# Performance work log

Hardware: AMD Instinct MI355X
Metric: run time of the kernel (lower is better)

## Reference

```python
import jax, jax.numpy as jnp
import numpy as np

B, T, I, H = 64, 256, 1024, 512


def _gru_layer(x, w_ih, w_hh, b_ih, b_hh):
    """PyTorch-semantics GRU layer, batch_first, h0=0.
    x: [B, T, In]; w_ih: [3H, In]; w_hh: [3H, H]; biases: [3H].
    Gate order (torch): r, z, n.
    """
    h_dim = w_hh.shape[1]
    # precompute input projections for all timesteps: [B, T, 3H]
    gx = jnp.einsum('bti,gi->btg', x, w_ih) + b_ih

    def step(h, gx_t):
        gh = h @ w_hh.T + b_hh                      # [B, 3H]
        xr, xz, xn = jnp.split(gx_t, 3, axis=-1)
        hr, hz, hn = jnp.split(gh, 3, axis=-1)
        r = jax.nn.sigmoid(xr + hr)
        z = jax.nn.sigmoid(xz + hz)
        n = jnp.tanh(xn + r * hn)
        h_new = (1.0 - z) * n + z * h
        return h_new, h_new

    h0 = jnp.zeros((x.shape[0], h_dim), x.dtype)
    _, out = jax.lax.scan(step, h0, jnp.swapaxes(gx, 0, 1))  # out: [T, B, H]
    return jnp.swapaxes(out, 0, 1)                            # [B, T, H]


def setup_inputs() -> dict:
    key = jax.random.key(0)
    ks = jax.random.split(key, 9)
    s1 = 1.0 / np.sqrt(H)   # torch GRU init: U(-1/sqrt(H), 1/sqrt(H)) of layer's hidden
    s2 = 1.0 / np.sqrt(I)
    u = lambda k, shp, s: jax.random.uniform(k, shp, jnp.float32, -s, s)
    return {
        'x': jax.random.normal(ks[0], (B, T, I), jnp.float32),
        'w_ih1': u(ks[1], (3 * H, I), s1),
        'w_hh1': u(ks[2], (3 * H, H), s1),
        'b_ih1': u(ks[3], (3 * H,), s1),
        'b_hh1': u(ks[4], (3 * H,), s1),
        'w_ih2': u(ks[5], (3 * I, H), s2),
        'w_hh2': u(ks[6], (3 * I, I), s2),
        'b_ih2': u(ks[7], (3 * I,), s2),
        'b_hh2': u(ks[8], (3 * I,), s2),
    }


def reference(x, w_ih1, w_hh1, b_ih1, b_hh1, w_ih2, w_hh2, b_ih2, b_hh2):
    h1 = _gru_layer(x, w_ih1, w_hh1, b_ih1, b_hh1)   # [B, T, H]
    h1 = jax.nn.relu(h1)
    out = _gru_layer(h1, w_ih2, w_hh2, b_ih2, b_hh2)  # [B, T, I]
    return out
```

## Files before the change

kernel.cpp:

```cpp
#include <hip/hip_runtime.h>

typedef _Float16 half_t;
typedef _Float16 half8  __attribute__((ext_vector_type(8)));
typedef _Float16 half4v __attribute__((ext_vector_type(4)));
typedef float    f32x4  __attribute__((ext_vector_type(4)));
typedef int      i32x4  __attribute__((ext_vector_type(4)));

#define NB 64
#define NT 256
#define NI 1024
#define NH 512

__device__ __forceinline__ void gload16_cc(i32x4& v, const void* p) {
    asm volatile("global_load_dwordx4 %0, %1, off sc0 sc1"
                 : "=v"(v) : "v"(p) : "memory");
}
__device__ __forceinline__ void gstore16_cc(void* p, i32x4 v) {
    asm volatile("global_store_dwordx4 %0, %1, off sc0 sc1"
                 :: "v"(p), "v"(v) : "memory");
}

__device__ __forceinline__ void flag_barrier(unsigned* slots, int nslots,
                                             int my, unsigned gen, int tid) {
    if (tid < 64) {
        asm volatile("s_waitcnt vmcnt(0)" ::: "memory");
        if (tid == 0) {
            unsigned gv = gen;
            asm volatile("global_store_dword %0, %1, off sc0 sc1"
                         :: "v"(slots + my), "v"(gv) : "memory");
        }
        const unsigned* p = slots + (tid & (nslots - 1));
        int guard = 0;
        while (true) {
            unsigned v;
            asm volatile("global_load_dword %0, %1, off sc0 sc1"
                         : "=v"(v) : "v"(p) : "memory");
            asm volatile("s_waitcnt vmcnt(0)" ::: "memory");
            if (__all(v >= gen)) break;
            __builtin_amdgcn_s_sleep(1);
            if (++guard > (1 << 22)) break;
        }
    }
    __syncthreads();
}

__global__ __launch_bounds__(256) void k_cvt(const float* __restrict__ s,
                                             half_t* __restrict__ d, int n4) {
    int i = blockIdx.x * 256 + threadIdx.x;
    if (i < n4) {
        float4 v = reinterpret_cast<const float4*>(s)[i];
        half4v h;
        h[0] = (half_t)v.x; h[1] = (half_t)v.y; h[2] = (half_t)v.z; h[3] = (half_t)v.w;
        reinterpret_cast<half4v*>(d)[i] = h;
    }
}

template <int K>
__global__ __launch_bounds__(256) void k_gemm(const half_t* __restrict__ A,
                                              const half_t* __restrict__ Bw,
                                              const float* __restrict__ bias,
                                              half_t* __restrict__ C, int N) {
    constexpr int BK = 64;
    __shared__ half_t Al[2][128 * BK] __attribute__((aligned(16)));
    __shared__ half_t Bl[2][128 * BK] __attribute__((aligned(16)));

    const int tid = threadIdx.x, lane = tid & 63, wv = tid >> 6;
    const long m0 = (long)blockIdx.y * 128;
    const long n0 = (long)blockIdx.x * 128;
    const int wm = (wv >> 1) * 64, wn = (wv & 1) * 64;

    f32x4 acc[4][4];
#pragma unroll
    for (int nt = 0; nt < 4; ++nt) {
        float bv = bias[n0 + wn + nt * 16 + (lane & 15)];
#pragma unroll
        for (int mt = 0; mt < 4; ++mt) acc[mt][nt] = (f32x4){bv, bv, bv, bv};
    }

    auto stage = [&](int buf, int kt) {
#pragma unroll
        for (int j = 0; j < 4; ++j) {
            int c = tid + 256 * j;
            int row = c >> 3, cin = c & 7;
            int dst = row * BK + ((cin ^ (row & 7)) << 3);
            *reinterpret_cast<int4*>(&Al[buf][dst]) =
                *reinterpret_cast<const int4*>(A + (m0 + row) * K + kt * BK + cin * 8);
            *reinterpret_cast<int4*>(&Bl[buf][dst]) =
                *reinterpret_cast<const int4*>(Bw + (n0 + row) * K + kt * BK + cin * 8);
        }
    };

    stage(0, 0);
    __syncthreads();
    constexpr int NK = K / BK;
    int buf = 0;
    for (int kt = 0; kt < NK; ++kt) {
        if (kt + 1 < NK) stage(buf ^ 1, kt + 1);
        half8 af[4][2], bf[4][2];
#pragma unroll
        for (int mt = 0; mt < 4; ++mt)
#pragma unroll
            for (int ks = 0; ks < 2; ++ks) {
                int lr = wm + mt * 16 + (lane & 15);
                int off = lr * BK + ((ks * 32 + 8 * (lane >> 4)) ^ ((lr & 7) << 3));
                af[mt][ks] = *reinterpret_cast<const half8*>(&Al[buf][off]);
            }
#pragma unroll
        for (int nt = 0; nt < 4; ++nt)
#pragma unroll
            for (int ks = 0; ks < 2; ++ks) {
                int lr = wn + nt * 16 + (lane & 15);
                int off = lr * BK + ((ks * 32 + 8 * (lane >> 4)) ^ ((lr & 7) << 3));
                bf[nt][ks] = *reinterpret_cast<const half8*>(&Bl[buf][off]);
            }
#pragma unroll
        for (int mt = 0; mt < 4; ++mt)
#pragma unroll
            for (int nt = 0; nt < 4; ++nt)
#pragma unroll
                for (int ks = 0; ks < 2; ++ks)
                    acc[mt][nt] = __builtin_amdgcn_mfma_f32_16x16x32_f16(
                        af[mt][ks], bf[nt][ks], acc[mt][nt], 0, 0, 0);
        __syncthreads();
        buf ^= 1;
    }
#pragma unroll
    for (int mt = 0; mt < 4; ++mt)
#pragma unroll
        for (int nt = 0; nt < 4; ++nt)
#pragma unroll
            for (int i = 0; i < 4; ++i) {
                long row = m0 + wm + mt * 16 + 4 * (lane >> 4) + i;
                long col = n0 + wn + nt * 16 + (lane & 15);
                C[row * N + col] = (half_t)acc[mt][nt][i];
            }
}

__global__ __launch_bounds__(256, 1) void k_phase1(const half_t* __restrict__ whh,
                                                   const float* __restrict__ bhh,
                                                   const half_t* __restrict__ gx,
                                                   half_t* __restrict__ hrelu,
                                                   half_t* __restrict__ hf16,
                                                   unsigned* __restrict__ slots) {
    __shared__ half_t wl[48 * NH] __attribute__((aligned(16)));
    __shared__ half_t hl[16 * NH] __attribute__((aligned(16)));
    __shared__ float xch[3][8][16];
    __shared__ half_t hstore[8][16] __attribute__((aligned(16)));

    const int tid = threadIdx.x, lane = tid & 63, wv = tid >> 6;
    const int g = blockIdx.x & 7, memb = blockIdx.x >> 3;
    const int e0 = memb * 16;
    unsigned* gslots = slots + g * 64;

#pragma unroll
    for (int j = 0; j < 12; ++j) {
        int c = tid + 256 * j;
        int lr = c >> 6, cin = c & 63;
        int grow = (lr >> 4) * NH + e0 + (lr & 15);
        int dst = lr * NH + ((cin ^ (lr & 7)) << 3);
        *reinterpret_cast<int4*>(&wl[dst]) =
            *reinterpret_cast<const int4*>(whh + (long)grow * NH + cin * 8);
    }
#pragma unroll
    for (int j = 0; j < 2; ++j) {
        int c = tid + 256 * j;
        int lr = 8 + (c >> 6), cin = c & 63;
        int4 z; z.x = z.y = z.z = z.w = 0;
        *reinterpret_cast<int4*>(&hl[lr * NH + cin * 8]) = z;
    }
    if (tid < 16) {
        i32x4 z = (i32x4){0, 0, 0, 0};
        int b = tid >> 1, seg = tid & 1;
        gstore16_cc(hf16 + (g * 8 + b) * NH + e0 + seg * 8, z);
    }
    float hp = 0.f;
    __syncthreads();
    flag_barrier(gslots, 32, memb, 1, tid);

    const float bgate = (wv < 3) ? bhh[wv * NH + e0 + (lane & 15)] : 0.f;
    const int b = tid >> 4, e = tid & 15;

    for (int t = 0; t < NT; ++t) {
        const half_t* hsrc = hf16 + (t & 1) * (NB * NH);
        i32x4 sv[2];
#pragma unroll
        for (int j = 0; j < 2; ++j) {
            int c = tid + 256 * j;
            int lr = c >> 6, cin = c & 63;
            gload16_cc(sv[j], hsrc + (g * 8 + lr) * NH + cin * 8);
        }
        float xr = 0.f, xz = 0.f, xn = 0.f;
        long rowbase = 0;
        if (tid < 128) {
            rowbase = (long)(g * 8 + b) * NT + t;
            long gbase = rowbase * (3 * NH) + e0 + e;
            xr = (float)gx[gbase];
            xz = (float)gx[gbase + NH];
            xn = (float)gx[gbase + 2 * NH];
        }
        asm volatile("s_waitcnt vmcnt(0)" ::: "memory");
#pragma unroll
        for (int j = 0; j < 2; ++j) {
            int c = tid + 256 * j;
            int lr = c >> 6, cin = c & 63;
            *reinterpret_cast<i32x4*>(&hl[lr * NH + ((cin ^ (lr & 7)) << 3)]) = sv[j];
        }
        __syncthreads();

        if (wv < 3) {
            f32x4 a0 = (f32x4){bgate, bgate, bgate, bgate};
            f32x4 a1 = (f32x4){0.f, 0.f, 0.f, 0.f};
#pragma unroll
            for (int ks = 0; ks < 16; ks += 2) {
                int ar = lane & 15;
                int br = wv * 16 + (lane & 15);
                int ao0 = ar * NH + ((ks * 32 + 8 * (lane >> 4)) ^ ((ar & 7) << 3));
                int bo0 = br * NH + ((ks * 32 + 8 * (lane >> 4)) ^ ((br & 7) << 3));
                int ao1 = ar * NH + (((ks + 1) * 32 + 8 * (lane >> 4)) ^ ((ar & 7) << 3));
                int bo1 = br * NH + (((ks + 1) * 32 + 8 * (lane >> 4)) ^ ((br & 7) << 3));
                a0 = __builtin_amdgcn_mfma_f32_16x16x32_f16(
                    *reinterpret_cast<const half8*>(&hl[ao0]),
                    *reinterpret_cast<const half8*>(&wl[bo0]), a0, 0, 0, 0);
                a1 = __builtin_amdgcn_mfma_f32_16x16x32_f16(
                    *reinterpret_cast<const half8*>(&hl[ao1]),
                    *reinterpret_cast<const half8*>(&wl[bo1]), a1, 0, 0, 0);
            }
            f32x4 acc = a0 + a1;
            if (lane < 32) {
#pragma unroll
                for (int i = 0; i < 4; ++i)
                    xch[wv][4 * (lane >> 4) + i][lane & 15] = acc[i];
            }
        }
        __syncthreads();

        if (tid < 128) {
            float r = 1.f / (1.f + __expf(-(xr + xch[0][b][e])));
            float z = 1.f / (1.f + __expf(-(xz + xch[1][b][e])));
            float n = tanhf(xn + r * xch[2][b][e]);
            float hn = (1.f - z) * n + z * hp;
            hp = hn;
            hrelu[rowbase * NH + e0 + e] = (half_t)fmaxf(hn, 0.f);
            hstore[b][e] = (half_t)hn;
        }
        __syncthreads();

        if (t + 1 < NT) {
            if (tid < 16) {
                int bb = tid >> 1, seg = tid & 1;
                i32x4 v = *reinterpret_cast<const i32x4*>(&hstore[bb][seg * 8]);
                gstore16_cc(hf16 + ((t + 1) & 1) * (NB * NH) + (g * 8 + bb) * NH + e0 + seg * 8, v);
            }
            flag_barrier(gslots, 32, memb, t + 2, tid);
        }
    }
}

__global__ __launch_bounds__(256, 1) void k_phase2(const half_t* __restrict__ whh,
                                                   const float* __restrict__ bhh,
                                                   const half_t* __restrict__ gx,
                                                   float* __restrict__ out,
                                                   half_t* __restrict__ hf16,
                                                   unsigned* __restrict__ slots) {
    __shared__ half_t wl[48 * NI] __attribute__((aligned(16)));
    __shared__ half_t hl[16 * NI] __attribute__((aligned(16)));
    __shared__ float xch[3][16][16];
    __shared__ half_t hstore[16][16] __attribute__((aligned(16)));

    const int tid = threadIdx.x, lane = tid & 63, wv = tid >> 6;
    const int xcd = blockIdx.x & 7;
    const int g = xcd >> 1;
    const int memb = ((blockIdx.x >> 3) << 1) | (xcd & 1);
    const int e0 = memb * 16;
    unsigned* gslots = slots + g * 64;

#pragma unroll
    for (int j = 0; j < 24; ++j) {
        int c = tid + 256 * j;
        int lr = c >> 7, cin = c & 127;
        int grow = (lr >> 4) * NI + e0 + (lr & 15);
        int dst = lr * NI + ((cin ^ (lr & 7)) << 3);
        *reinterpret_cast<int4*>(&wl[dst]) =
            *reinterpret_cast<const int4*>(whh + (long)grow * NI + cin * 8);
    }
    if (tid < 32) {
        i32x4 z = (i32x4){0, 0, 0, 0};
        int b = tid >> 1, seg = tid & 1;
        gstore16_cc(hf16 + (g * 16 + b) * NI + e0 + seg * 8, z);
    }
    float hp = 0.f;
    __syncthreads();
    flag_barrier(gslots, 64, memb, 1, tid);

    const float bgate = (wv < 3) ? bhh[wv * NI + e0 + (lane & 15)] : 0.f;
    const int b = tid >> 4, e = tid & 15;

    for (int t = 0; t < NT; ++t) {
        const half_t* hsrc = hf16 + (t & 1) * (NB * NI);
        i32x4 sv[8];
#pragma unroll
        for (int j = 0; j < 8; ++j) {
            int c = tid + 256 * j;
            int lr = c >> 7, cin = c & 127;
            gload16_cc(sv[j], hsrc + (g * 16 + lr) * NI + cin * 8);
        }
        long rowbase = (long)(g * 16 + b) * NT + t;
        long gbase = rowbase * (3 * NI) + e0 + e;
        float xr = (float)gx[gbase];
        float xz = (float)gx[gbase + NI];
        float xn = (float)gx[gbase + 2 * NI];
        asm volatile("s_waitcnt vmcnt(0)" ::: "memory");
#pragma unroll
        for (int j = 0; j < 8; ++j) {
            int c = tid + 256 * j;
            int lr = c >> 7, cin = c & 127;
            *reinterpret_cast<i32x4*>(&hl[lr * NI + ((cin ^ (lr & 7)) << 3)]) = sv[j];
        }
        __syncthreads();

        if (wv < 3) {
            f32x4 a0 = (f32x4){bgate, bgate, bgate, bgate};
            f32x4 a1 = (f32x4){0.f, 0.f, 0.f, 0.f};
#pragma unroll
            for (int ks = 0; ks < 32; ks += 2) {
                int ar = lane & 15;
                int br = wv * 16 + (lane & 15);
                int ao0 = ar * NI + ((ks * 32 + 8 * (lane >> 4)) ^ ((ar & 7) << 3));
                int bo0 = br * NI + ((ks * 32 + 8 * (lane >> 4)) ^ ((br & 7) << 3));
                int ao1 = ar * NI + (((ks + 1) * 32 + 8 * (lane >> 4)) ^ ((ar & 7) << 3));
                int bo1 = br * NI + (((ks + 1) * 32 + 8 * (lane >> 4)) ^ ((br & 7) << 3));
                a0 = __builtin_amdgcn_mfma_f32_16x16x32_f16(
                    *reinterpret_cast<const half8*>(&hl[ao0]),
                    *reinterpret_cast<const half8*>(&wl[bo0]), a0, 0, 0, 0);
                a1 = __builtin_amdgcn_mfma_f32_16x16x32_f16(
                    *reinterpret_cast<const half8*>(&hl[ao1]),
                    *reinterpret_cast<const half8*>(&wl[bo1]), a1, 0, 0, 0);
            }
            f32x4 acc = a0 + a1;
#pragma unroll
            for (int i = 0; i < 4; ++i)
                xch[wv][4 * (lane >> 4) + i][lane & 15] = acc[i];
        }
        __syncthreads();

        {
            float r = 1.f / (1.f + __expf(-(xr + xch[0][b][e])));
            float z = 1.f / (1.f + __expf(-(xz + xch[1][b][e])));
            float n = tanhf(xn + r * xch[2][b][e]);
            float hn = (1.f - z) * n + z * hp;
            hp = hn;
            out[rowbase * NI + e0 + e] = hn;
            hstore[b][e] = (half_t)hn;
        }
        __syncthreads();

        if (t + 1 < NT) {
            if (tid < 32) {
                int bb = tid >> 1, seg = tid & 1;
                i32x4 v = *reinterpret_cast<const i32x4*>(&hstore[bb][seg * 8]);
                gstore16_cc(hf16 + ((t + 1) & 1) * (NB * NI) + (g * 16 + bb) * NI + e0 + seg * 8, v);
            }
            flag_barrier(gslots, 64, memb, t + 2, tid);
        }
    }
}

extern "C" void kernel_launch(void* const* d_in, const int* in_sizes, int n_in,
                              void* d_out, int out_size, void* d_ws, size_t ws_size,
                              hipStream_t stream) {
    const float* x     = (const float*)d_in[0];
    const float* w_ih1 = (const float*)d_in[1];
    const float* w_hh1 = (const float*)d_in[2];
    const float* b_ih1 = (const float*)d_in[3];
    const float* b_hh1 = (const float*)d_in[4];
    const float* w_ih2 = (const float*)d_in[5];
    const float* w_hh2 = (const float*)d_in[6];
    const float* b_ih2 = (const float*)d_in[7];
    const float* b_hh2 = (const float*)d_in[8];

    char* ws = (char*)d_ws;
    unsigned* slots1 = (unsigned*)ws;
    unsigned* slots2 = (unsigned*)(ws + 2048);
    half_t* h1f16  = (half_t*)(ws + 4096);
    half_t* h2f16  = (half_t*)(ws + 266240);
    half_t* wih1h  = (half_t*)(ws + 1048576);
    half_t* whh1h  = (half_t*)(ws + 4194304);
    half_t* wih2h  = (half_t*)(ws + 5767168);
    half_t* whh2h  = (half_t*)(ws + 8912896);
    half_t* xh     = (half_t*)(ws + 16777216);
    half_t* hrelu  = (half_t*)(ws + 16777216);
    half_t* gx1    = (half_t*)(ws + 50331648);
    half_t* gx2    = (half_t*)(ws + 50331648);
    float*  out    = (float*)d_out;

    hipMemsetAsync(ws, 0, 4096, stream);

    k_cvt<<<16384, 256, 0, stream>>>(x,     xh,    4194304);
    k_cvt<<<1536,  256, 0, stream>>>(w_ih1, wih1h, 393216);
    k_cvt<<<768,   256, 0, stream>>>(w_hh1, whh1h, 196608);
    k_cvt<<<1536,  256, 0, stream>>>(w_ih2, wih2h, 393216);
    k_cvt<<<3072,  256, 0, stream>>>(w_hh2, whh2h, 786432);

    k_gemm<1024><<<dim3(12, 128), 256, 0, stream>>>(xh, wih1h, b_ih1, gx1, 1536);
    k_phase1<<<256, 256, 0, stream>>>(whh1h, b_hh1, gx1, hrelu, h1f16, slots1);
    k_gemm<512><<<dim3(24, 128), 256, 0, stream>>>(hrelu, wih2h, b_ih2, gx2, 3072);
    k_phase2<<<256, 256, 0, stream>>>(whh2h, b_hh2, gx2, out, h2f16, slots2);
}
```

Measured before the change: 2.139 ms.

## Fuse layer-2 input projection into layer-1 recurrence and convert x inside GEMM

The separate x conversion kernel is removed. The first GEMM now reads fp32 x and converts it to fp16 while staging tiles into shared memory. The layer-2 input projection GEMM and the relu buffer are removed: in phase1 the otherwise idle fourth wave applies relu to the previous step's hidden state and multiplies it by a per-block slice of w_ih2, writing gx2 into a shared buffer that aliases gx1. Both recurrent kernels now prefetch the next step's gate inputs, and phase2 moves its output store between the flag release and the wait. This removes kernel launches and the hrelu round trip, but adds per-step work and LDS use to the latency-bound recurrence, and relies on in-place aliasing of gx1 and gx2 being safe.

```diff
diff --git a/kernel.cpp b/kernel.cpp
--- a/kernel.cpp
+++ b/kernel.cpp
@@ -2,7 +2,6 @@
 
 typedef _Float16 half_t;
 typedef _Float16 half8  __attribute__((ext_vector_type(8)));
-typedef _Float16 half4v __attribute__((ext_vector_type(4)));
 typedef float    f32x4  __attribute__((ext_vector_type(4)));
 typedef int      i32x4  __attribute__((ext_vector_type(4)));
 
@@ -49,17 +48,16 @@
     int i = blockIdx.x * 256 + threadIdx.x;
     if (i < n4) {
         float4 v = reinterpret_cast<const float4*>(s)[i];
-        half4v h;
-        h[0] = (half_t)v.x; h[1] = (half_t)v.y; h[2] = (half_t)v.z; h[3] = (half_t)v.w;
-        reinterpret_cast<half4v*>(d)[i] = h;
-    }
-}
-
-template <int K>
-__global__ __launch_bounds__(256) void k_gemm(const half_t* __restrict__ A,
+        half_t h4[4] = {(half_t)v.x, (half_t)v.y, (half_t)v.z, (half_t)v.w};
+        *reinterpret_cast<long*>(&d[i * 4]) = *reinterpret_cast<long*>(h4);
+    }
+}
+
+template <int K, bool AF32>
+__global__ __launch_bounds__(256) void k_gemm(const void* __restrict__ Av,
                                               const half_t* __restrict__ Bw,
                                               const float* __restrict__ bias,
-                                              half_t* __restrict__ C, int N) {
+                                              half_t* __restrict__ C, int N, int ldc) {
     constexpr int BK = 64;
     __shared__ half_t Al[2][128 * BK] __attribute__((aligned(16)));
     __shared__ half_t Bl[2][128 * BK] __attribute__((aligned(16)));
@@ -83,8 +81,20 @@
             int c = tid + 256 * j;
             int row = c >> 3, cin = c & 7;
             int dst = row * BK + ((cin ^ (row & 7)) << 3);
-            *reinterpret_cast<int4*>(&Al[buf][dst]) =
-                *reinterpret_cast<const int4*>(A + (m0 + row) * K + kt * BK + cin * 8);
+            if constexpr (AF32) {
+                const float* Af = (const float*)Av;
+                const float* src = Af + (m0 + row) * K + kt * BK + cin * 8;
+                float4 f0 = *reinterpret_cast<const float4*>(src);
+                float4 f1 = *reinterpret_cast<const float4*>(src + 4);
+                half8 h;
+                h[0] = (half_t)f0.x; h[1] = (half_t)f0.y; h[2] = (half_t)f0.z; h[3] = (half_t)f0.w;
+                h[4] = (half_t)f1.x; h[5] = (half_t)f1.y; h[6] = (half_t)f1.z; h[7] = (half_t)f1.w;
+                *reinterpret_cast<half8*>(&Al[buf][dst]) = h;
+            } else {
+                const half_t* Ah = (const half_t*)Av;
+                *reinterpret_cast<int4*>(&Al[buf][dst]) =
+                    *reinterpret_cast<const int4*>(Ah + (m0 + row) * K + kt * BK + cin * 8);
+            }
             *reinterpret_cast<int4*>(&Bl[buf][dst]) =
                 *reinterpret_cast<const int4*>(Bw + (n0 + row) * K + kt * BK + cin * 8);
         }
@@ -132,20 +142,26 @@
             for (int i = 0; i < 4; ++i) {
                 long row = m0 + wm + mt * 16 + 4 * (lane >> 4) + i;
                 long col = n0 + wn + nt * 16 + (lane & 15);
-                C[row * N + col] = (half_t)acc[mt][nt][i];
-            }
-}
+                C[row * (long)ldc + col] = (half_t)acc[mt][nt][i];
+            }
+}
+
+#define XCH(gt, bb, ee) xch[((gt) * 8 + (bb)) * 16 + (ee)]
 
 __global__ __launch_bounds__(256, 1) void k_phase1(const half_t* __restrict__ whh,
                                                    const float* __restrict__ bhh,
-                                                   const half_t* __restrict__ gx,
-                                                   half_t* __restrict__ hrelu,
+                                                   const half_t* gx,
+                                                   const half_t* __restrict__ wih2,
+                                                   const float* __restrict__ bih2,
+                                                   half_t* gx2,
                                                    half_t* __restrict__ hf16,
                                                    unsigned* __restrict__ slots) {
-    __shared__ half_t wl[48 * NH] __attribute__((aligned(16)));
-    __shared__ half_t hl[16 * NH] __attribute__((aligned(16)));
-    __shared__ float xch[3][8][16];
-    __shared__ half_t hstore[8][16] __attribute__((aligned(16)));
+    __shared__ __attribute__((aligned(16))) char arena[163840];
+    half_t* wl  = (half_t*)arena;
+    half_t* wl2 = (half_t*)(arena + 49152);
+    half_t* hl  = (half_t*)(arena + 147456);
+    float*  xch = (float*)(arena + 147456 + 8192);
+    half_t* hst = (half_t*)(arena + 147456 + 8192 + 1536);
 
     const int tid = threadIdx.x, lane = tid & 63, wv = tid >> 6;
     const int g = blockIdx.x & 7, memb = blockIdx.x >> 3;
@@ -162,23 +178,37 @@
             *reinterpret_cast<const int4*>(whh + (long)grow * NH + cin * 8);
     }
 #pragma unroll
-    for (int j = 0; j < 2; ++j) {
+    for (int j = 0; j < 24; ++j) {
         int c = tid + 256 * j;
-        int lr = 8 + (c >> 6), cin = c & 63;
-        int4 z; z.x = z.y = z.z = z.w = 0;
-        *reinterpret_cast<int4*>(&hl[lr * NH + cin * 8]) = z;
+        int lr = c >> 6, cin = c & 63;
+        int dst = lr * NH + ((cin ^ (lr & 7)) << 3);
+        *reinterpret_cast<int4*>(&wl2[dst]) =
+            *reinterpret_cast<const int4*>(wih2 + (long)(memb * 96 + lr) * NH + cin * 8);
     }
     if (tid < 16) {
         i32x4 z = (i32x4){0, 0, 0, 0};
-        int b = tid >> 1, seg = tid & 1;
-        gstore16_cc(hf16 + (g * 8 + b) * NH + e0 + seg * 8, z);
+        int bb = tid >> 1, seg = tid & 1;
+        gstore16_cc(hf16 + (g * 8 + bb) * NH + e0 + seg * 8, z);
     }
     float hp = 0.f;
     __syncthreads();
     flag_barrier(gslots, 32, memb, 1, tid);
 
     const float bgate = (wv < 3) ? bhh[wv * NH + e0 + (lane & 15)] : 0.f;
+    float bg2[6];
+    if (wv == 3) {
+#pragma unroll
+        for (int nt2 = 0; nt2 < 6; ++nt2)
+            bg2[nt2] = bih2[memb * 96 + nt2 * 16 + (lane & 15)];
+    }
     const int b = tid >> 4, e = tid & 15;
+    const long rb0 = (long)(g * 8 + b) * NT;
+
+    float xr = 0.f, xz = 0.f, xn = 0.f, nxr = 0.f, nxz = 0.f, nxn = 0.f;
+    if (tid < 128) {
+        long gb = rb0 * 3072 + e0 + e;
+        xr = (float)gx[gb]; xz = (float)gx[gb + NH]; xn = (float)gx[gb + 2 * NH];
+    }
 
     for (int t = 0; t < NT; ++t) {
         const half_t* hsrc = hf16 + (t & 1) * (NB * NH);
@@ -189,15 +219,6 @@
             int lr = c >> 6, cin = c & 63;
             gload16_cc(sv[j], hsrc + (g * 8 + lr) * NH + cin * 8);
         }
-        float xr = 0.f, xz = 0.f, xn = 0.f;
-        long rowbase = 0;
-        if (tid < 128) {
-            rowbase = (long)(g * 8 + b) * NT + t;
-            long gbase = rowbase * (3 * NH) + e0 + e;
-            xr = (float)gx[gbase];
-            xz = (float)gx[gbase + NH];
-            xn = (float)gx[gbase + 2 * NH];
-        }
         asm volatile("s_waitcnt vmcnt(0)" ::: "memory");
 #pragma unroll
         for (int j = 0; j < 2; ++j) {
@@ -206,6 +227,11 @@
             *reinterpret_cast<i32x4*>(&hl[lr * NH + ((cin ^ (lr & 7)) << 3)]) = sv[j];
         }
         __syncthreads();
+
+        if (tid < 128 && t + 1 < NT) {
+            long gb = (rb0 + t + 1) * 3072 + e0 + e;
+            nxr = (float)gx[gb]; nxz = (float)gx[gb + NH]; nxn = (float)gx[gb + 2 * NH];
+        }
 
         if (wv < 3) {
             f32x4 a0 = (f32x4){bgate, bgate, bgate, bgate};
@@ -229,29 +255,111 @@
             if (lane < 32) {
 #pragma unroll
                 for (int i = 0; i < 4; ++i)
-                    xch[wv][4 * (lane >> 4) + i][lane & 15] = acc[i];
+                    XCH(wv, 4 * (lane >> 4) + i, lane & 15) = acc[i];
+            }
+        } else if (t > 0) {
+            f32x4 g2[6];
+#pragma unroll
+            for (int nt2 = 0; nt2 < 6; ++nt2)
+                g2[nt2] = (f32x4){bg2[nt2], bg2[nt2], bg2[nt2], bg2[nt2]};
+#pragma unroll
+            for (int ks = 0; ks < 16; ++ks) {
+                int ar = lane & 15;
+                int ao = ar * NH + ((ks * 32 + 8 * (lane >> 4)) ^ ((ar & 7) << 3));
+                half8 a = *reinterpret_cast<const half8*>(&hl[ao]);
+#pragma unroll
+                for (int j2 = 0; j2 < 8; ++j2)
+                    a[j2] = a[j2] > (half_t)0.f ? a[j2] : (half_t)0.f;
+#pragma unroll
+                for (int nt2 = 0; nt2 < 6; ++nt2) {
+                    int br2 = nt2 * 16 + (lane & 15);
+                    int bo = br2 * NH + ((ks * 32 + 8 * (lane >> 4)) ^ ((br2 & 7) << 3));
+                    g2[nt2] = __builtin_amdgcn_mfma_f32_16x16x32_f16(
+                        a, *reinterpret_cast<const half8*>(&wl2[bo]), g2[nt2], 0, 0, 0);
+                }
+            }
+            if (lane < 32) {
+                int r0 = 4 * (lane >> 4);
+#pragma unroll
+                for (int nt2 = 0; nt2 < 6; ++nt2)
+#pragma unroll
+                    for (int i = 0; i < 4; ++i) {
+                        long bb = g * 8 + r0 + i;
+                        gx2[(bb * NT + (t - 1)) * 3072 + memb * 96 + nt2 * 16 + (lane & 15)] =
+                            (half_t)g2[nt2][i];
+                    }
             }
         }
         __syncthreads();
 
         if (tid < 128) {
-            float r = 1.f / (1.f + __expf(-(xr + xch[0][b][e])));
-            float z = 1.f / (1.f + __expf(-(xz + xch[1][b][e])));
-            float n = tanhf(xn + r * xch[2][b][e]);
+            float r = 1.f / (1.f + __expf(-(xr + XCH(0, b, e))));
+            float z = 1.f / (1.f + __expf(-(xz + XCH(1, b, e))));
+            float n = tanhf(xn + r * XCH(2, b, e));
             float hn = (1.f - z) * n + z * hp;
             hp = hn;
-            hrelu[rowbase * NH + e0 + e] = (half_t)fmaxf(hn, 0.f);
-            hstore[b][e] = (half_t)hn;
-        }
-        __syncthreads();
-
-        if (t + 1 < NT) {
-            if (tid < 16) {
-                int bb = tid >> 1, seg = tid & 1;
-                i32x4 v = *reinterpret_cast<const i32x4*>(&hstore[bb][seg * 8]);
-                gstore16_cc(hf16 + ((t + 1) & 1) * (NB * NH) + (g * 8 + bb) * NH + e0 + seg * 8, v);
-            }
-            flag_barrier(gslots, 32, memb, t + 2, tid);
+            hst[b * 16 + e] = (half_t)hn;
+        }
+        __syncthreads();
+
+        if (tid < 16) {
+            int bb = tid >> 1, seg = tid & 1;
+            i32x4 v = *reinterpret_cast<const i32x4*>(&hst[bb * 16 + seg * 8]);
+            gstore16_cc(hf16 + ((t + 1) & 1) * (NB * NH) + (g * 8 + bb) * NH + e0 + seg * 8, v);
+        }
+        flag_barrier(gslots, 32, memb, t + 2, tid);
+        xr = nxr; xz = nxz; xn = nxn;
+    }
+
+    {
+        const half_t* hsrc = hf16 + (NT & 1) * (NB * NH);
+        i32x4 sv[2];
+#pragma unroll
+        for (int j = 0; j < 2; ++j) {
+            int c = tid + 256 * j;
+            int lr = c >> 6, cin = c & 63;
+            gload16_cc(sv[j], hsrc + (g * 8 + lr) * NH + cin * 8);
+        }
+        asm volatile("s_waitcnt vmcnt(0)" ::: "memory");
+#pragma unroll
+        for (int j = 0; j < 2; ++j) {
+            int c = tid + 256 * j;
+            int lr = c >> 6, cin = c & 63;
+            *reinterpret_cast<i32x4*>(&hl[lr * NH + ((cin ^ (lr & 7)) << 3)]) = sv[j];
+        }
+        __syncthreads();
+        if (wv == 3) {
+            f32x4 g2[6];
+#pragma unroll
+            for (int nt2 = 0; nt2 < 6; ++nt2)
+                g2[nt2] = (f32x4){bg2[nt2], bg2[nt2], bg2[nt2], bg2[nt2]};
+#pragma unroll
+            for (int ks = 0; ks < 16; ++ks) {
+                int ar = lane & 15;
+                int ao = ar * NH + ((ks * 32 + 8 * (lane >> 4)) ^ ((ar & 7) << 3));
+                half8 a = *reinterpret_cast<const half8*>(&hl[ao]);
+#pragma unroll
+                for (int j2 = 0; j2 < 8; ++j2)
+                    a[j2] = a[j2] > (half_t)0.f ? a[j2] : (half_t)0.f;
+#pragma unroll
+                for (int nt2 = 0; nt2 < 6; ++nt2) {
+                    int br2 = nt2 * 16 + (lane & 15);
+                    int bo = br2 * NH + ((ks * 32 + 8 * (lane >> 4)) ^ ((br2 & 7) << 3));
+                    g2[nt2] = __builtin_amdgcn_mfma_f32_16x16x32_f16(
+                        a, *reinterpret_cast<const half8*>(&wl2[bo]), g2[nt2], 0, 0, 0);
+                }
+            }
+            if (lane < 32) {
+                int r0 = 4 * (lane >> 4);
+#pragma unroll
+                for (int nt2 = 0; nt2 < 6; ++nt2)
+#pragma unroll
+                    for (int i = 0; i < 4; ++i) {
+                        long bb = g * 8 + r0 + i;
+                        gx2[(bb * NT + (NT - 1)) * 3072 + memb * 96 + nt2 * 16 + (lane & 15)] =
+                            (half_t)g2[nt2][i];
+                    }
+            }
         }
     }
 }
@@ -264,8 +372,8 @@
                                                    unsigned* __restrict__ slots) {
     __shared__ half_t wl[48 * NI] __attribute__((aligned(16)));
     __shared__ half_t hl[16 * NI] __attribute__((aligned(16)));
-    __shared__ float xch[3][16][16];
-    __shared__ half_t hstore[16][16] __attribute__((aligned(16)));
+    __shared__ float xch2[3][16][16];
+    __shared__ half_t hst[16][16] __attribute__((aligned(16)));
 
     const int tid = threadIdx.x, lane = tid & 63, wv = tid >> 6;
     const int xcd = blockIdx.x & 7;
@@ -285,8 +393,8 @@
     }
     if (tid < 32) {
         i32x4 z = (i32x4){0, 0, 0, 0};
-        int b = tid >> 1, seg = tid & 1;
-        gstore16_cc(hf16 + (g * 16 + b) * NI + e0 + seg * 8, z);
+        int bb = tid >> 1, seg = tid & 1;
+        gstore16_cc(hf16 + (g * 16 + bb) * NI + e0 + seg * 8, z);
     }
     float hp = 0.f;
     __syncthreads();
@@ -294,6 +402,13 @@
 
     const float bgate = (wv < 3) ? bhh[wv * NI + e0 + (lane & 15)] : 0.f;
     const int b = tid >> 4, e = tid & 15;
+    const long rb0 = (long)(g * 16 + b) * NT;
+
+    float xr, xz, xn, nxr = 0.f, nxz = 0.f, nxn = 0.f;
+    {
+        long gb = rb0 * 3072 + e0 + e;
+        xr = (float)gx[gb]; xz = (float)gx[gb + NI]; xn = (float)gx[gb + 2 * NI];
+    }
 
     for (int t = 0; t < NT; ++t) {
         const half_t* hsrc = hf16 + (t & 1) * (NB * NI);
@@ -304,11 +419,6 @@
             int lr = c >> 7, cin = c & 127;
             gload16_cc(sv[j], hsrc + (g * 16 + lr) * NI + cin * 8);
         }
-        long rowbase = (long)(g * 16 + b) * NT + t;
-        long gbase = rowbase * (3 * NI) + e0 + e;
-        float xr = (float)gx[gbase];
-        float xz = (float)gx[gbase + NI];
-        float xn = (float)gx[gbase + 2 * NI];
         asm volatile("s_waitcnt vmcnt(0)" ::: "memory");
 #pragma unroll
         for (int j = 0; j < 8; ++j) {
@@ -317,6 +427,11 @@
             *reinterpret_cast<i32x4*>(&hl[lr * NI + ((cin ^ (lr & 7)) << 3)]) = sv[j];
         }
         __syncthreads();
+
+        if (t + 1 < NT) {
+            long gb = (rb0 + t + 1) * 3072 + e0 + e;
+            nxr = (float)gx[gb]; nxz = (float)gx[gb + NI]; nxn = (float)gx[gb + 2 * NI];
+        }
 
         if (wv < 3) {
             f32x4 a0 = (f32x4){bgate, bgate, bgate, bgate};
@@ -339,29 +454,54 @@
             f32x4 acc = a0 + a1;
 #pragma unroll
             for (int i = 0; i < 4; ++i)
-                xch[wv][4 * (lane >> 4) + i][lane & 15] = acc[i];
-        }
-        __syncthreads();
-
+                xch2[wv][4 * (lane >> 4) + i][lane & 15] = acc[i];
+        }
+        __syncthreads();
+
+        float hn;
         {
-            float r = 1.f / (1.f + __expf(-(xr + xch[0][b][e])));
-            float z = 1.f / (1.f + __expf(-(xz + xch[1][b][e])));
-            float n = tanhf(xn + r * xch[2][b][e]);
-            float hn = (1.f - z) * n + z * hp;
+            float r = 1.f / (1.f + __expf(-(xr + xch2[0][b][e])));
+            float z = 1.f / (1.f + __expf(-(xz + xch2[1][b][e])));
+            float n = tanhf(xn + r * xch2[2][b][e]);
+            hn = (1.f - z) * n + z * hp;
             hp = hn;
-            out[rowbase * NI + e0 + e] = hn;
-            hstore[b][e] = (half_t)hn;
+            hst[b][e] = (half_t)hn;
         }
         __syncthreads();
 
         if (t + 1 < NT) {
             if (tid < 32) {
                 int bb = tid >> 1, seg = tid & 1;
-                i32x4 v = *reinterpret_cast<const i32x4*>(&hstore[bb][seg * 8]);
+                i32x4 v = *reinterpret_cast<const i32x4*>(&hst[bb][seg * 8]);
                 gstore16_cc(hf16 + ((t + 1) & 1) * (NB * NI) + (g * 16 + bb) * NI + e0 + seg * 8, v);
             }
-            flag_barrier(gslots, 64, memb, t + 2, tid);
-        }
+            if (tid < 64) {
+                asm volatile("s_waitcnt vmcnt(0)" ::: "memory");
+                if (tid == 0) {
+                    unsigned gv = t + 2;
+                    asm volatile("global_store_dword %0, %1, off sc0 sc1"
+                                 :: "v"(gslots + memb), "v"(gv) : "memory");
+                }
+            }
+        }
+        out[(rb0 + t) * NI + e0 + e] = hn;
+        if (t + 1 < NT) {
+            if (tid < 64) {
+                const unsigned* p = gslots + (tid & 63);
+                int guard = 0;
+                while (true) {
+                    unsigned v;
+                    asm volatile("global_load_dword %0, %1, off sc0 sc1"
+                                 : "=v"(v) : "v"(p) : "memory");
+                    asm volatile("s_waitcnt vmcnt(0)" ::: "memory");
+                    if (__all(v >= (unsigned)(t + 2))) break;
+                    __builtin_amdgcn_s_sleep(1);
+                    if (++guard > (1 << 22)) break;
+                }
+            }
+            __syncthreads();
+        }
+        xr = nxr; xz = nxz; xn = nxn;
     }
 }
 
@@ -382,27 +522,22 @@
     unsigned* slots1 = (unsigned*)ws;
     unsigned* slots2 = (unsigned*)(ws + 2048);
     half_t* h1f16  = (half_t*)(ws + 4096);
-    half_t* h2f16  = (half_t*)(ws + 266240);
+    half_t* h2f16  = (half_t*)(ws + 135168);
     half_t* wih1h  = (half_t*)(ws + 1048576);
     half_t* whh1h  = (half_t*)(ws + 4194304);
     half_t* wih2h  = (half_t*)(ws + 5767168);
     half_t* whh2h  = (half_t*)(ws + 8912896);
-    half_t* xh     = (half_t*)(ws + 16777216);
-    half_t* hrelu  = (half_t*)(ws + 16777216);
-    half_t* gx1    = (half_t*)(ws + 50331648);
-    half_t* gx2    = (half_t*)(ws + 50331648);
+    half_t* gxU    = (half_t*)(ws + 16777216);
     float*  out    = (float*)d_out;
 
     hipMemsetAsync(ws, 0, 4096, stream);
 
-    k_cvt<<<16384, 256, 0, stream>>>(x,     xh,    4194304);
-    k_cvt<<<1536,  256, 0, stream>>>(w_ih1, wih1h, 393216);
-    k_cvt<<<768,   256, 0, stream>>>(w_hh1, whh1h, 196608);
-    k_cvt<<<1536,  256, 0, stream>>>(w_ih2, wih2h, 393216);
-    k_cvt<<<3072,  256, 0, stream>>>(w_hh2, whh2h, 786432);
-
-    k_gemm<1024><<<dim3(12, 128), 256, 0, stream>>>(xh, wih1h, b_ih1, gx1, 1536);
-    k_phase1<<<256, 256, 0, stream>>>(whh1h, b_hh1, gx1, hrelu, h1f16, slots1);
-    k_gemm<512><<<dim3(24, 128), 256, 0, stream>>>(hrelu, wih2h, b_ih2, gx2, 3072);
-    k_phase2<<<256, 256, 0, stream>>>(whh2h, b_hh2, gx2, out, h2f16, slots2);
-}
+    k_cvt<<<1536, 256, 0, stream>>>(w_ih1, wih1h, 393216);
+    k_cvt<<<768,  256, 0, stream>>>(w_hh1, whh1h, 196608);
+    k_cvt<<<1536, 256, 0, stream>>>(w_ih2, wih2h, 393216);
+    k_cvt<<<3072, 256, 0, stream>>>(w_hh2, whh2h, 786432);
+
+    k_gemm<1024, true><<<dim3(12, 128), 256, 0, stream>>>(x, wih1h, b_ih1, gxU, 1536, 3072);
+    k_phase1<<<256, 256, 0, stream>>>(whh1h, b_hh1, gxU, wih2h, b_ih2, gxU, h1f16, slots1);
+    k_phase2<<<256, 256, 0, stream>>>(whh2h, b_hh2, gxU, out, h2f16, slots2);
+}
```

New measurement: 2.707 ms. +26.5%, slower.

## Fuse x fp32 conversion into GEMM, prefetch gate inputs and defer output stores

Applied to the files above, without the earlier changes.

Drops the separate conversion pass over x by converting fp32 to fp16 while staging the first input-projection GEMM. In both recurrent kernels, the next timestep's gx values are loaded during the current step, and the per-step output or ReLU stores are postponed to the start of the next iteration, keeping global-memory latency off the serialized recurrence. The spin barrier no longer sleeps between polls, which can cut wake-up latency but adds memory traffic. Risks include higher register pressure and heavier polling contention.

```diff
diff --git a/kernel.cpp b/kernel.cpp
--- a/kernel.cpp
+++ b/kernel.cpp
@@ -2,7 +2,6 @@
 
 typedef _Float16 half_t;
 typedef _Float16 half8  __attribute__((ext_vector_type(8)));
-typedef _Float16 half4v __attribute__((ext_vector_type(4)));
 typedef float    f32x4  __attribute__((ext_vector_type(4)));
 typedef int      i32x4  __attribute__((ext_vector_type(4)));
 
@@ -37,8 +36,7 @@
                          : "=v"(v) : "v"(p) : "memory");
             asm volatile("s_waitcnt vmcnt(0)" ::: "memory");
             if (__all(v >= gen)) break;
-            __builtin_amdgcn_s_sleep(1);
-            if (++guard > (1 << 22)) break;
+            if (++guard > (1 << 24)) break;
         }
     }
     __syncthreads();
@@ -49,17 +47,16 @@
     int i = blockIdx.x * 256 + threadIdx.x;
     if (i < n4) {
         float4 v = reinterpret_cast<const float4*>(s)[i];
-        half4v h;
-        h[0] = (half_t)v.x; h[1] = (half_t)v.y; h[2] = (half_t)v.z; h[3] = (half_t)v.w;
-        reinterpret_cast<half4v*>(d)[i] = h;
-    }
-}
-
-template <int K>
-__global__ __launch_bounds__(256) void k_gemm(const half_t* __restrict__ A,
+        half_t h4[4] = {(half_t)v.x, (half_t)v.y, (half_t)v.z, (half_t)v.w};
+        *reinterpret_cast<long*>(&d[i * 4]) = *reinterpret_cast<long*>(h4);
+    }
+}
+
+template <int K, bool AF32>
+__global__ __launch_bounds__(256) void k_gemm(const void* __restrict__ Av,
                                               const half_t* __restrict__ Bw,
                                               const float* __restrict__ bias,
-                                              half_t* __restrict__ C, int N) {
+                                              half_t* __restrict__ C, int N, int ldc) {
     constexpr int BK = 64;
     __shared__ half_t Al[2][128 * BK] __attribute__((aligned(16)));
     __shared__ half_t Bl[2][128 * BK] __attribute__((aligned(16)));
@@ -83,8 +80,20 @@
             int c = tid + 256 * j;
             int row = c >> 3, cin = c & 7;
             int dst = row * BK + ((cin ^ (row & 7)) << 3);
-            *reinterpret_cast<int4*>(&Al[buf][dst]) =
-                *reinterpret_cast<const int4*>(A + (m0 + row) * K + kt * BK + cin * 8);
+            if constexpr (AF32) {
+                const float* Af = (const float*)Av;
+                const float* src = Af + (m0 + row) * K + kt * BK + cin * 8;
+                float4 f0 = *reinterpret_cast<const float4*>(src);
+                float4 f1 = *reinterpret_cast<const float4*>(src + 4);
+                half8 h;
+                h[0] = (half_t)f0.x; h[1] = (half_t)f0.y; h[2] = (half_t)f0.z; h[3] = (half_t)f0.w;
+                h[4] = (half_t)f1.x; h[5] = (half_t)f1.y; h[6] = (half_t)f1.z; h[7] = (half_t)f1.w;
+                *reinterpret_cast<half8*>(&Al[buf][dst]) = h;
+            } else {
+                const half_t* Ah = (const half_t*)Av;
+                *reinterpret_cast<int4*>(&Al[buf][dst]) =
+                    *reinterpret_cast<const int4*>(Ah + (m0 + row) * K + kt * BK + cin * 8);
+            }
             *reinterpret_cast<int4*>(&Bl[buf][dst]) =
                 *reinterpret_cast<const int4*>(Bw + (n0 + row) * K + kt * BK + cin * 8);
         }
@@ -132,7 +141,7 @@
             for (int i = 0; i < 4; ++i) {
                 long row = m0 + wm + mt * 16 + 4 * (lane >> 4) + i;
                 long col = n0 + wn + nt * 16 + (lane & 15);
-                C[row * N + col] = (half_t)acc[mt][nt][i];
+                C[row * (long)ldc + col] = (half_t)acc[mt][nt][i];
             }
 }
 
@@ -145,7 +154,7 @@
     __shared__ half_t wl[48 * NH] __attribute__((aligned(16)));
     __shared__ half_t hl[16 * NH] __attribute__((aligned(16)));
     __shared__ float xch[3][8][16];
-    __shared__ half_t hstore[8][16] __attribute__((aligned(16)));
+    __shared__ half_t hst[8][16] __attribute__((aligned(16)));
 
     const int tid = threadIdx.x, lane = tid & 63, wv = tid >> 6;
     const int g = blockIdx.x & 7, memb = blockIdx.x >> 3;
@@ -170,17 +179,27 @@
     }
     if (tid < 16) {
         i32x4 z = (i32x4){0, 0, 0, 0};
-        int b = tid >> 1, seg = tid & 1;
-        gstore16_cc(hf16 + (g * 8 + b) * NH + e0 + seg * 8, z);
-    }
-    float hp = 0.f;
+        int bb = tid >> 1, seg = tid & 1;
+        gstore16_cc(hf16 + (g * 8 + bb) * NH + e0 + seg * 8, z);
+    }
+    float hp = 0.f, hrp = 0.f;
     __syncthreads();
     flag_barrier(gslots, 32, memb, 1, tid);
 
     const float bgate = (wv < 3) ? bhh[wv * NH + e0 + (lane & 15)] : 0.f;
     const int b = tid >> 4, e = tid & 15;
+    const long rb0 = (long)(g * 8 + b) * NT;
+
+    float xr = 0.f, xz = 0.f, xn = 0.f, nxr = 0.f, nxz = 0.f, nxn = 0.f;
+    if (tid < 128) {
+        long gb = rb0 * 1536 + e0 + e;
+        xr = (float)gx[gb]; xz = (float)gx[gb + NH]; xn = (float)gx[gb + 2 * NH];
+    }
 
     for (int t = 0; t < NT; ++t) {
+        if (tid < 128 && t > 0)
+            hrelu[(rb0 + t - 1) * NH + e0 + e] = (half_t)hrp;
+
         const half_t* hsrc = hf16 + (t & 1) * (NB * NH);
         i32x4 sv[2];
 #pragma unroll
@@ -189,15 +208,6 @@
             int lr = c >> 6, cin = c & 63;
             gload16_cc(sv[j], hsrc + (g * 8 + lr) * NH + cin * 8);
         }
-        float xr = 0.f, xz = 0.f, xn = 0.f;
-        long rowbase = 0;
-        if (tid < 128) {
-            rowbase = (long)(g * 8 + b) * NT + t;
-            long gbase = rowbase * (3 * NH) + e0 + e;
-            xr = (float)gx[gbase];
-            xz = (float)gx[gbase + NH];
-            xn = (float)gx[gbase + 2 * NH];
-        }
         asm volatile("s_waitcnt vmcnt(0)" ::: "memory");
 #pragma unroll
         for (int j = 0; j < 2; ++j) {
@@ -206,6 +216,11 @@
             *reinterpret_cast<i32x4*>(&hl[lr * NH + ((cin ^ (lr & 7)) << 3)]) = sv[j];
         }
         __syncthreads();
+
+        if (tid < 128 && t + 1 < NT) {
+            long gb = (rb0 + t + 1) * 1536 + e0 + e;
+            nxr = (float)gx[gb]; nxz = (float)gx[gb + NH]; nxn = (float)gx[gb + 2 * NH];
+        }
 
         if (wv < 3) {
             f32x4 a0 = (f32x4){bgate, bgate, bgate, bgate};
@@ -240,20 +255,23 @@
             float n = tanhf(xn + r * xch[2][b][e]);
             float hn = (1.f - z) * n + z * hp;
             hp = hn;
-            hrelu[rowbase * NH + e0 + e] = (half_t)fmaxf(hn, 0.f);
-            hstore[b][e] = (half_t)hn;
+            hrp = fmaxf(hn, 0.f);
+            hst[b][e] = (half_t)hn;
         }
         __syncthreads();
 
         if (t + 1 < NT) {
             if (tid < 16) {
                 int bb = tid >> 1, seg = tid & 1;
-                i32x4 v = *reinterpret_cast<const i32x4*>(&hstore[bb][seg * 8]);
+                i32x4 v = *reinterpret_cast<const i32x4*>(&hst[bb][seg * 8]);
                 gstore16_cc(hf16 + ((t + 1) & 1) * (NB * NH) + (g * 8 + bb) * NH + e0 + seg * 8, v);
             }
             flag_barrier(gslots, 32, memb, t + 2, tid);
         }
-    }
+        xr = nxr; xz = nxz; xn = nxn;
+    }
+    if (tid < 128)
+        hrelu[(rb0 + NT - 1) * NH + e0 + e] = (half_t)hrp;
 }
 
 __global__ __launch_bounds__(256, 1) void k_phase2(const half_t* __restrict__ whh,
@@ -264,8 +282,8 @@
                                                    unsigned* __restrict__ slots) {
     __shared__ half_t wl[48 * NI] __attribute__((aligned(16)));
     __shared__ half_t hl[16 * NI] __attribute__((aligned(16)));
-    __shared__ float xch[3][16][16];
-    __shared__ half_t hstore[16][16] __attribute__((aligned(16)));
+    __shared__ float xch2[3][16][16];
+    __shared__ half_t hst[16][16] __attribute__((aligned(16)));
 
     const int tid = threadIdx.x, lane = tid & 63, wv = tid >> 6;
     const int xcd = blockIdx.x & 7;
@@ -285,8 +303,8 @@
     }
     if (tid < 32) {
         i32x4 z = (i32x4){0, 0, 0, 0};
-        int b = tid >> 1, seg = tid & 1;
-        gstore16_cc(hf16 + (g * 16 + b) * NI + e0 + seg * 8, z);
+        int bb = tid >> 1, seg = tid & 1;
+        gstore16_cc(hf16 + (g * 16 + bb) * NI + e0 + seg * 8, z);
     }
     float hp = 0.f;
     __syncthreads();
@@ -294,8 +312,18 @@
 
     const float bgate = (wv < 3) ? bhh[wv * NI + e0 + (lane & 15)] : 0.f;
     const int b = tid >> 4, e = tid & 15;
+    const long rb0 = (long)(g * 16 + b) * NT;
+
+    float xr, xz, xn, nxr = 0.f, nxz = 0.f, nxn = 0.f;
+    {
+        long gb = rb0 * 3072 + e0 + e;
+        xr = (float)gx[gb]; xz = (float)gx[gb + NI]; xn = (float)gx[gb + 2 * NI];
+    }
 
     for (int t = 0; t < NT; ++t) {
+        if (t > 0)
+            out[(rb0 + t - 1) * NI + e0 + e] = hp;
+
         const half_t* hsrc = hf16 + (t & 1) * (NB * NI);
         i32x4 sv[8];
 #pragma unroll
@@ -304,11 +332,6 @@
             int lr = c >> 7, cin = c & 127;
             gload16_cc(sv[j], hsrc + (g * 16 + lr) * NI + cin * 8);
         }
-        long rowbase = (long)(g * 16 + b) * NT + t;
-        long gbase = rowbase * (3 * NI) + e0 + e;
-        float xr = (float)gx[gbase];
-        float xz = (float)gx[gbase + NI];
-        float xn = (float)gx[gbase + 2 * NI];
         asm volatile("s_waitcnt vmcnt(0)" ::: "memory");
 #pragma unroll
         for (int j = 0; j < 8; ++j) {
@@ -317,6 +340,11 @@
             *reinterpret_cast<i32x4*>(&hl[lr * NI + ((cin ^ (lr & 7)) << 3)]) = sv[j];
         }
         __syncthreads();
+
+        if (t + 1 < NT) {
+            long gb = (rb0 + t + 1) * 3072 + e0 + e;
+            nxr = (float)gx[gb]; nxz = (float)gx[gb + NI]; nxn = (float)gx[gb + 2 * NI];
+        }
 
         if (wv < 3) {
             f32x4 a0 = (f32x4){bgate, bgate, bgate, bgate};
@@ -339,30 +367,31 @@
             f32x4 acc = a0 + a1;
 #pragma unroll
             for (int i = 0; i < 4; ++i)
-                xch[wv][4 * (lane >> 4) + i][lane & 15] = acc[i];
+                xch2[wv][4 * (lane >> 4) + i][lane & 15] = acc[i];
         }
         __syncthreads();
 
         {
-            float r = 1.f / (1.f + __expf(-(xr + xch[0][b][e])));
-            float z = 1.f / (1.f + __expf(-(xz + xch[1][b][e])));
-            float n = tanhf(xn + r * xch[2][b][e]);
+            float r = 1.f / (1.f + __expf(-(xr + xch2[0][b][e])));
+            float z = 1.f / (1.f + __expf(-(xz + xch2[1][b][e])));
+            float n = tanhf(xn + r * xch2[2][b][e]);
             float hn = (1.f - z) * n + z * hp;
             hp = hn;
-            out[rowbase * NI + e0 + e] = hn;
-            hstore[b][e] = (half_t)hn;
+            hst[b][e] = (half_t)hn;
         }
         __syncthreads();
 
         if (t + 1 < NT) {
             if (tid < 32) {
                 int bb = tid >> 1, seg = tid & 1;
-                i32x4 v = *reinterpret_cast<const i32x4*>(&hstore[bb][seg * 8]);
+                i32x4 v = *reinterpret_cast<const i32x4*>(&hst[bb][seg * 8]);
                 gstore16_cc(hf16 + ((t + 1) & 1) * (NB * NI) + (g * 16 + bb) * NI + e0 + seg * 8, v);
             }
             flag_barrier(gslots, 64, memb, t + 2, tid);
         }
-    }
+        xr = nxr; xz = nxz; xn = nxn;
+    }
+    out[(rb0 + NT - 1) * NI + e0 + e] = hp;
 }
 
 extern "C" void kernel_launch(void* const* d_in, const int* in_sizes, int n_in,
@@ -382,27 +411,24 @@
     unsigned* slots1 = (unsigned*)ws;
     unsigned* slots2 = (unsigned*)(ws + 2048);
     half_t* h1f16  = (half_t*)(ws + 4096);
-    half_t* h2f16  = (half_t*)(ws + 266240);
+    half_t* h2f16  = (half_t*)(ws + 135168);
     half_t* wih1h  = (half_t*)(ws + 1048576);
     half_t* whh1h  = (half_t*)(ws + 4194304);
     half_t* wih2h  = (half_t*)(ws + 5767168);
     half_t* whh2h  = (half_t*)(ws + 8912896);
-    half_t* xh     = (half_t*)(ws + 16777216);
     half_t* hrelu  = (half_t*)(ws + 16777216);
-    half_t* gx1    = (half_t*)(ws + 50331648);
-    half_t* gx2    = (half_t*)(ws + 50331648);
+    half_t* gxU    = (half_t*)(ws + 50331648);
     float*  out    = (float*)d_out;
 
     hipMemsetAsync(ws, 0, 4096, stream);
 
-    k_cvt<<<16384, 256, 0, stream>>>(x,     xh,    4194304);
-    k_cvt<<<1536,  256, 0, stream>>>(w_ih1, wih1h, 393216);
-    k_cvt<<<768,   256, 0, stream>>>(w_hh1, whh1h, 196608);
-    k_cvt<<<1536,  256, 0, stream>>>(w_ih2, wih2h, 393216);
-    k_cvt<<<3072,  256, 0, stream>>>(w_hh2, whh2h, 786432);
-
-    k_gemm<1024><<<dim3(12, 128), 256, 0, stream>>>(xh, wih1h, b_ih1, gx1, 1536);
-    k_phase1<<<256, 256, 0, stream>>>(whh1h, b_hh1, gx1, hrelu, h1f16, slots1);
-    k_gemm<512><<<dim3(24, 128), 256, 0, stream>>>(hrelu, wih2h, b_ih2, gx2, 3072);
-    k_phase2<<<256, 256, 0, stream>>>(whh2h, b_hh2, gx2, out, h2f16, slots2);
-}
+    k_cvt<<<1536, 256, 0, stream>>>(w_ih1, wih1h, 393216);
+    k_cvt<<<768,  256, 0, stream>>>(w_hh1, whh1h, 196608);
+    k_cvt<<<1536, 256, 0, stream>>>(w_ih2, wih2h, 393216);
+    k_cvt<<<3072, 256, 0, stream>>>(w_hh2, whh2h, 786432);
+
+    k_gemm<1024, true><<<dim3(12, 128), 256, 0, stream>>>(x, wih1h, b_ih1, gxU, 1536, 1536);
+    k_phase1<<<256, 256, 0, stream>>>(whh1h, b_hh1, gxU, hrelu, h1f16, slots1);
+    k_gemm<512, false><<<dim3(24, 128), 256, 0, stream>>>(hrelu, wih2h, b_ih2, gxU, 3072, 3072);
+    k_phase2<<<256, 256, 0, stream>>>(whh2h, b_hh2, gxU, out, h2f16, slots2);
+}
```

Result: slower. 2.533 ms (+18.4%).
